# Performance work log

Measured on AMD Instinct MI355X. Metric: run time of the kernel, lower is better.

Reference implementation:

```python
import jax, jax.numpy as jnp
import numpy as np


def _patch_size(w):
    # mirrors PatchLoss size selection (static shape -> Python branch is fine)
    if w == 512:
        return 64
    elif 256 <= w < 512:
        return 32
    raise ValueError('error size')


def setup_inputs() -> dict:
    key = jax.random.key(0)
    k1, k2 = jax.random.split(key)
    shape = (1, 3, 32, 512, 512)  # (b=1, c, t, h, w)
    x = jax.random.normal(k1, shape, dtype=jnp.float32)
    x_r = jax.random.normal(k2, shape, dtype=jnp.float32)
    return {"x": x, "x_r": x_r}


def reference(x, x_r):
    _, c, t, h, w = x.shape
    size = _patch_size(w)
    tc, hc, wc = 1, size // 2, size // 2
    # L = |(x+1)/2 - (x_r+1)/2| ; original detaches before pooling
    L = jnp.abs((x + 1.0) / 2.0 - (x_r + 1.0) / 2.0)
    D = jax.lax.stop_gradient(L)[0]  # (c, t, h, w), batch squeezed
    # patch means over (c, hc, wc) for each frame (tc=1) and spatial block
    nh, nw = h // hc, w // wc
    P = D.reshape(c, t, nh, hc, nw, wc).mean(axis=(0, 3, 5))  # (t, nh, nw)
    # max over spatial patches; original init max_patch=0.0, so clamp at 0
    max_patches = jnp.maximum(P.max(axis=(1, 2)), 0.0)  # (t,)
    return jnp.log(max_patches.mean())
```

## Files before the change

kernel.cpp:

```cpp
#include <hip/hip_runtime.h>
#include <math.h>


typedef float vf4 __attribute__((ext_vector_type(4)));

__global__ __launch_bounds__(256) void patch_sum_kernel(
    const float* __restrict__ x, const float* __restrict__ xr,
    float* __restrict__ part) {
  const int b   = blockIdx.x;
  const int tid = threadIdx.x;
  const vf4* __restrict__ a4 = (const vf4*)x  + (size_t)b * 2048;
  const vf4* __restrict__ c4 = (const vf4*)xr + (size_t)b * 2048;

  float s0 = 0.f, s1 = 0.f, s2 = 0.f, s3 = 0.f;
#pragma unroll
  for (int i = 0; i < 8; ++i) {
    vf4 a = __builtin_nontemporal_load(&a4[i * 256 + tid]);
    vf4 c = __builtin_nontemporal_load(&c4[i * 256 + tid]);
    s0 += fabsf(a.x - c.x);
    s1 += fabsf(a.y - c.y);
    s2 += fabsf(a.z - c.z);
    s3 += fabsf(a.w - c.w);
  }
  float acc = (s0 + s1) + (s2 + s3);

  acc += __shfl_down(acc, 4, 8);
  acc += __shfl_down(acc, 2, 8);
  acc += __shfl_down(acc, 1, 8);
  __shared__ float s[32];
  if ((tid & 7) == 0) s[tid >> 3] = acc;
  __syncthreads();
  if (tid < 16) part[(size_t)b * 16 + tid] = s[tid] + s[tid + 16];
}

__global__ __launch_bounds__(1024) void finalize_kernel(
    const float* __restrict__ part, float* __restrict__ out) {
  const int tid = threadIdx.x;
  const int t = tid >> 5;
  const int j = tid & 31;
  float m = -1e30f;
#pragma unroll
  for (int k = 0; k < 8; ++k) {
    int p = t * 256 + j + 32 * k;
    int ph = (p >> 4) & 15;
    int pw = p & 15;
    float v = 0.f;
#pragma unroll
    for (int ch = 0; ch < 3; ++ch) {
#pragma unroll
      for (int half = 0; half < 2; ++half) {
        int idx = ((ch << 10) + (t << 5) + (ph << 1) + half) * 16 + pw;
        v += part[idx];
      }
    }
    m = fmaxf(m, v);
  }
#pragma unroll
  for (int o = 16; o > 0; o >>= 1) m = fmaxf(m, __shfl_down(m, o, 32));
  __shared__ float s[32];
  if (j == 0) s[t] = fmaxf(m * (0.5f / 3072.0f), 0.f);
  __syncthreads();
  if (tid < 32) {
    float v = s[tid];
#pragma unroll
    for (int o = 16; o > 0; o >>= 1) v += __shfl_down(v, o, 32);
    if (tid == 0) out[0] = logf(v * (1.0f / 32.0f));
  }
}

extern "C" void kernel_launch(void* const* d_in, const int* in_sizes, int n_in,
                              void* d_out, int out_size, void* d_ws, size_t ws_size,
                              hipStream_t stream) {
  const float* x  = (const float*)d_in[0];
  const float* xr = (const float*)d_in[1];
  float* part = (float*)d_ws;
  float* out  = (float*)d_out;

  patch_sum_kernel<<<3072, 256, 0, stream>>>(x, xr, part);
  finalize_kernel<<<1, 1024, 0, stream>>>(part, out);
}
```

Measured before the change: 194.2 us.

## Stream inputs via global_load_lds into LDS and halve per-block work

Each block now covers half as many rows: one wave's worth of 4 KB per tensor per iteration, copied with direct global-to-LDS loads, after which threads read back from shared memory. The grid doubles to 6144 blocks, and the finalize kernel sums four partial rows per patch row instead of two. The aim is to raise the number of memory requests in flight and take the load traffic off VGPRs. In exchange it adds 32 KB of LDS per block, which may cap occupancy, plus a full waitcnt with no overlap inside each block.

```diff
diff --git a/kernel.cpp b/kernel.cpp
--- a/kernel.cpp
+++ b/kernel.cpp
@@ -1,22 +1,43 @@
 #include <hip/hip_runtime.h>
 #include <math.h>
+#include <stdint.h>
 
 
 typedef float vf4 __attribute__((ext_vector_type(4)));
+typedef __attribute__((address_space(1))) const void gas_void;
+typedef __attribute__((address_space(3))) void lds_void;
 
 __global__ __launch_bounds__(256) void patch_sum_kernel(
     const float* __restrict__ x, const float* __restrict__ xr,
     float* __restrict__ part) {
+  __shared__ vf4 ldsA[1024];
+  __shared__ vf4 ldsC[1024];
   const int b   = blockIdx.x;
   const int tid = threadIdx.x;
-  const vf4* __restrict__ a4 = (const vf4*)x  + (size_t)b * 2048;
-  const vf4* __restrict__ c4 = (const vf4*)xr + (size_t)b * 2048;
+  const int wave = tid >> 6;
+  const int lane = tid & 63;
+
+  const vf4* a4 = (const vf4*)x  + (size_t)b * 1024;
+  const vf4* c4 = (const vf4*)xr + (size_t)b * 1024;
+
+#pragma unroll
+  for (int i = 0; i < 4; ++i) {
+    const int s = i * 4 + wave;
+    __builtin_amdgcn_global_load_lds(
+        (gas_void*)(uintptr_t)(a4 + (size_t)s * 64 + lane),
+        (lds_void*)(uintptr_t)(ldsA + s * 64), 16, 0, 2 );
+    __builtin_amdgcn_global_load_lds(
+        (gas_void*)(uintptr_t)(c4 + (size_t)s * 64 + lane),
+        (lds_void*)(uintptr_t)(ldsC + s * 64), 16, 0, 2 );
+  }
+  __builtin_amdgcn_s_waitcnt(0);
+  __builtin_amdgcn_sched_barrier(0);
 
   float s0 = 0.f, s1 = 0.f, s2 = 0.f, s3 = 0.f;
 #pragma unroll
-  for (int i = 0; i < 8; ++i) {
-    vf4 a = __builtin_nontemporal_load(&a4[i * 256 + tid]);
-    vf4 c = __builtin_nontemporal_load(&c4[i * 256 + tid]);
+  for (int i = 0; i < 4; ++i) {
+    vf4 a = ldsA[i * 256 + tid];
+    vf4 c = ldsC[i * 256 + tid];
     s0 += fabsf(a.x - c.x);
     s1 += fabsf(a.y - c.y);
     s2 += fabsf(a.z - c.z);
@@ -27,10 +48,10 @@
   acc += __shfl_down(acc, 4, 8);
   acc += __shfl_down(acc, 2, 8);
   acc += __shfl_down(acc, 1, 8);
-  __shared__ float s[32];
-  if ((tid & 7) == 0) s[tid >> 3] = acc;
+  __shared__ float sb[32];
+  if ((tid & 7) == 0) sb[tid >> 3] = acc;
   __syncthreads();
-  if (tid < 16) part[(size_t)b * 16 + tid] = s[tid] + s[tid + 16];
+  if (tid < 16) part[(size_t)b * 16 + tid] = sb[tid] + sb[tid + 16];
 }
 
 __global__ __launch_bounds__(1024) void finalize_kernel(
@@ -48,8 +69,8 @@
 #pragma unroll
     for (int ch = 0; ch < 3; ++ch) {
 #pragma unroll
-      for (int half = 0; half < 2; ++half) {
-        int idx = ((ch << 10) + (t << 5) + (ph << 1) + half) * 16 + pw;
+      for (int q = 0; q < 4; ++q) {
+        int idx = (ch * 2048 + t * 64 + ph * 4 + q) * 16 + pw;
         v += part[idx];
       }
     }
@@ -76,6 +97,6 @@
   float* part = (float*)d_ws;
   float* out  = (float*)d_out;
 
-  patch_sum_kernel<<<3072, 256, 0, stream>>>(x, xr, part);
+  patch_sum_kernel<<<6144, 256, 0, stream>>>(x, xr, part);
   finalize_kernel<<<1, 1024, 0, stream>>>(part, out);
 }
```

After: 196.5 us. Within noise of the previous version (+1.2%).
